# Kernel optimization log

Measured on AMD Instinct MI355X. Metric: run time of the kernel, lower is better.

Reference implementation:

```python
import jax, jax.numpy as jnp
import numpy as np

# ---- db4 filters (pywt conventions: dec_lo = rec_lo[::-1], rec_hi = qmf(rec_lo)) ----
F = 8  # db4 filter length
_rec_lo = np.array([0.23037781330885523, 0.7148465705525415, 0.6308807679295904,
                    -0.027983769416983849, -0.18703481171888114, 0.030841381835986965,
                    0.032883011666982945, -0.010597401784997278], dtype=np.float32)
_rec_hi = _rec_lo[::-1].copy()
_rec_hi[1::2] *= -1.0
REC_LO = jnp.asarray(_rec_lo)
REC_HI = jnp.asarray(_rec_hi)

MAX_LEVEL = 9  # pywt.dwt_max_level(4096, 8)


def _conv1d(x, kernel, stride=1, padding='VALID', lhs_dilation=None):
    # x: [B, L] -> correlation (XLA conv does NOT flip the kernel)
    out = jax.lax.conv_general_dilated(
        x[:, None, :], kernel[None, None, :],
        window_strides=(stride,), padding=padding,
        lhs_dilation=lhs_dilation,
        dimension_numbers=('NCH', 'OIH', 'NCH'))
    return out[:, 0, :]


def dwt(x):
    # pywt.dwt(x, 'db4', mode='symmetric'):
    # cA = np.convolve(sym_ext(x, F-1), dec_lo, 'valid')[1::2]
    # convolution with dec filter == correlation with rec filter (its reverse)
    ext = jnp.pad(x, ((0, 0), (F - 1, F - 1)), mode='symmetric')[:, 1:]
    return _conv1d(ext, REC_LO, stride=2), _conv1d(ext, REC_HI, stride=2)


def idwt(ca, cd):
    # pywt.idwt: zero-upsample coeffs, full convolution with rec filters, trim edges
    n = ca.shape[1]
    pad = ((F - 1, F - 1),)
    out = (_conv1d(ca, REC_LO[::-1], padding=pad, lhs_dilation=(2,)) +
           _conv1d(cd, REC_HI[::-1], padding=pad, lhs_dilation=(2,)))
    return out[:, F - 2:2 * n]  # output length = 2n - F + 2


def wavelet_features(x1):
    # Faithful to WaveletDWTLayer stack + WaveletParsingLayer: at each level k>=2,
    # reconstruct with details of levels k and k-1 only (others zeroed), with
    # pywt.waverec's trim-by-one rule; concatenate the 8 full-length reconstructions.
    a = x1
    cds, recs = [], []
    for level in range(1, MAX_LEVEL + 1):
        a, d = dwt(a)
        if level >= 2:
            r = idwt(jnp.zeros_like(d), d)
            for j in range(level - 2, -1, -1):
                dj = cds[j] if j == level - 2 else jnp.zeros_like(cds[j])
                if r.shape[1] == dj.shape[1] + 1:  # waverec trim rule
                    r = r[:, :-1]
                r = idwt(r, dj)
            recs.append(r)  # [B, signal_length]
        cds.append(d)
    return jnp.concatenate(recs, axis=1)  # [B, signal_length*(MAX_LEVEL-1)]


def reference(x1, x2, x3, W0, b0, W1, b1, W2, b2):
    # x2/x3 are placeholders in the original module (overwritten by layers 1/2)
    h = wavelet_features(x1)
    for W, b in ((W0, b0), (W1, b1), (W2, b2)):
        h = jax.nn.relu(h) @ W.T + b
    return h


def setup_inputs() -> dict:
    key = jax.random.key(0)
    ks = jax.random.split(key, 4)
    B, N = 2048, 4096
    D_IN, H1, H2, OUT = 32768, 181, 13, 10
    return {
        'x1': jax.random.normal(ks[0], (B, N), jnp.float32),
        'x2': jnp.zeros((B, 1, 8), jnp.float32),
        'x3': jnp.zeros((B, 1, 8), jnp.float32),
        'W0': jax.random.normal(ks[1], (H1, D_IN), jnp.float32) / np.float32(np.sqrt(D_IN)),
        'b0': jnp.zeros((H1,), jnp.float32),
        'W1': jax.random.normal(ks[2], (H2, H1), jnp.float32) / np.float32(np.sqrt(H1)),
        'b1': jnp.zeros((H2,), jnp.float32),
        'W2': jax.random.normal(ks[3], (OUT, H2), jnp.float32) / np.float32(np.sqrt(H2)),
        'b2': jnp.zeros((OUT,), jnp.float32),
    }
```

## Files before the change

kernel.cpp:

```cpp
#include <hip/hip_runtime.h>
#include <hip/hip_bf16.h>


typedef _Float16 f16x8 __attribute__((ext_vector_type(8)));
typedef _Float16 f16x4v __attribute__((ext_vector_type(4)));
typedef float f32x4 __attribute__((ext_vector_type(4)));

#define WV_THREADS 256
#define NSPLIT 32
#define KCHUNK 1024
#define GEMM_BM 256

#define L0 0.23037781330885523f
#define L1 0.7148465705525415f
#define L2f 0.6308807679295904f
#define L3 -0.02798376941698385f
#define L4 -0.18703481171888114f
#define L5 0.030841381835986965f
#define L6 0.032883011666982945f
#define L7 -0.010597401784997278f

#define H0 -0.010597401784997278f
#define H1 -0.032883011666982945f
#define H2 0.030841381835986965f
#define H3 0.18703481171888114f
#define H4 -0.02798376941698385f
#define H5 -0.6308807679295904f
#define H6 0.7148465705525415f
#define H7 -0.23037781330885523f

__constant__ constexpr int cNL[10] = {4096, 2051, 1029, 518, 262, 134, 70, 38, 22, 14};

__device__ __forceinline__ int ext_idx(int j, int n) {
  return (j < 6) ? (5 - j) : ((j < n + 6) ? (j - 6) : (2 * n + 5 - j));
}

__device__ __forceinline__ void dwt2(const float* a, float* anext, float* d,
                                     int n, int m, bool store_a) {
  const int ng = (m + 1) >> 1;
  for (int g = threadIdx.x; g < ng; g += WV_THREADS) {
    float w[10];
    if (g >= 2 && 4 * g + 9 <= n + 5) {
      const float2* af = (const float2*)a + (2 * g - 3);
      float2 b0 = af[0], b1 = af[1], b2 = af[2], b3 = af[3], b4 = af[4];
      w[0] = b0.x; w[1] = b0.y; w[2] = b1.x; w[3] = b1.y; w[4] = b2.x;
      w[5] = b2.y; w[6] = b3.x; w[7] = b3.y; w[8] = b4.x; w[9] = b4.y;
    } else {
#pragma unroll
      for (int q = 0; q < 10; ++q) {
        int j = 4 * g + q;
        int jm = n + 12;
        if (j > jm) j = jm;
        w[q] = a[ext_idx(j, n)];
      }
    }
    float sl0 = w[0]*L0 + w[1]*L1 + w[2]*L2f + w[3]*L3 + w[4]*L4 + w[5]*L5 + w[6]*L6 + w[7]*L7;
    float sh0 = w[0]*H0 + w[1]*H1 + w[2]*H2  + w[3]*H3 + w[4]*H4 + w[5]*H5 + w[6]*H6 + w[7]*H7;
    float sl1 = w[2]*L0 + w[3]*L1 + w[4]*L2f + w[5]*L3 + w[6]*L4 + w[7]*L5 + w[8]*L6 + w[9]*L7;
    float sh1 = w[2]*H0 + w[3]*H1 + w[4]*H2  + w[5]*H3 + w[6]*H4 + w[7]*H5 + w[8]*H6 + w[9]*H7;
    if (2 * g + 1 < m) {
      if (store_a) *(float2*)(anext + 2 * g) = make_float2(sl0, sl1);
      *(float2*)(d + 2 * g) = make_float2(sh0, sh1);
    } else {
      if (store_a) anext[2 * g] = sl0;
      d[2 * g] = sh0;
    }
  }
}

#define SWZ(u) ((u) ^ (((u) >> 3) & 7))
__device__ __forceinline__ const float4* lds4c(const float* b, int s) {
  return (const float4*)b + SWZ(s);
}
__device__ __forceinline__ float4* lds4(float* b, int s) {
  return (float4*)b + SWZ(s);
}

template <int NP>
__device__ __forceinline__ void lvlL(const float* a, float* v) {
#pragma unroll
  for (int q = 0; q < NP; ++q) {
    v[2*q]   = a[q+3]*L0 + a[q+2]*L2f + a[q+1]*L4 + a[q]*L6;
    v[2*q+1] = a[q+3]*L1 + a[q+2]*L3  + a[q+1]*L5 + a[q]*L7;
  }
}
template <int NP>
__device__ __forceinline__ void lvlH(const float* d, float* v) {
#pragma unroll
  for (int q = 0; q < NP; ++q) {
    v[2*q]   = d[q+3]*H0 + d[q+2]*H2 + d[q+1]*H4 + d[q]*H6;
    v[2*q+1] = d[q+3]*H1 + d[q+2]*H3 + d[q+1]*H5 + d[q]*H7;
  }
}
template <int NP>
__device__ __forceinline__ void lvlLH(const float* a, const float* d, float* v) {
#pragma unroll
  for (int q = 0; q < NP; ++q) {
    v[2*q]   = a[q+3]*L0 + a[q+2]*L2f + a[q+1]*L4 + a[q]*L6
             + d[q+3]*H0 + d[q+2]*H2  + d[q+1]*H4 + d[q]*H6;
    v[2*q+1] = a[q+3]*L1 + a[q+2]*L3  + a[q+1]*L5 + a[q]*L7
             + d[q+3]*H1 + d[q+2]*H3  + d[q+1]*H5 + d[q]*H7;
  }
}

__device__ __forceinline__ void g8f2(const float* p, int s, float* w) {
#pragma unroll
  for (int i = 0; i < 4; ++i) {
    float2 v = *(const float2*)(p + s + 2 * i);
    w[2*i] = v.x; w[2*i+1] = v.y;
  }
}
__device__ __forceinline__ void g12f4(const float* p, int s, float* w) {
#pragma unroll
  for (int i = 0; i < 3; ++i) {
    float4 v = *(const float4*)(p + s + 4 * i);
    w[4*i] = v.x; w[4*i+1] = v.y; w[4*i+2] = v.z; w[4*i+3] = v.w;
  }
}

__device__ __forceinline__ void store16(_Float16* outg, int t, const float* v) {
  f16x8 h0, h1;
#pragma unroll
  for (int i = 0; i < 8; ++i) h0[i] = (_Float16)fmaxf(v[i], 0.f);
#pragma unroll
  for (int i = 0; i < 8; ++i) h1[i] = (_Float16)fmaxf(v[8 + i], 0.f);
  *(f16x8*)(outg + 16 * t) = h0;
  *(f16x8*)(outg + 16 * t + 8) = h1;
}

__device__ __forceinline__ void fin2(const float* d2, const float* d1, _Float16* og) {
  const int t = threadIdx.x;
  float dw[12];  g12f4(d2, 4 * t, dw);
  float mid[12]; lvlH<6>(dw, mid);
  float d1w[12]; g12f4(d1, 8 * t, d1w);
  float v[16];   lvlLH<8>(mid, d1w, v);
  store16(og, t, v);
}

__device__ __forceinline__ void fin3(const float* d3, const float* d2, _Float16* og) {
  const int t = threadIdx.x;
  float dw[8];   g8f2(d3, 2 * t, dw);
  float v0[10];  lvlH<5>(dw, v0);
  float d2w[12]; g12f4(d2, 4 * t, d2w);
  float v1[12];  lvlLH<6>(v0, d2w, v1);
  float v[16];   lvlL<8>(v1, v);
  store16(og, t, v);
}

__device__ __forceinline__ void fin4(const float* d4, const float* d3, _Float16* og) {
  const int t = threadIdx.x;
  float dw[7];
#pragma unroll
  for (int i = 0; i < 7; ++i) dw[i] = d4[t + i];
  float v0[8];   lvlH<4>(dw, v0);
  float d3w[8];  g8f2(d3, 2 * t, d3w);
  float v1[10];  lvlLH<5>(v0, d3w, v1);
  float v2[12];  lvlL<6>(v1, v2);
  float v[16];   lvlL<8>(v2, v);
  store16(og, t, v);
}

template <bool FINAL, int N>
__device__ __forceinline__ void stepL(const float* ca, float* outl, _Float16* outg) {
  constexpr int npair = N - 3;
  constexpr int ng = (npair + 7) >> 3;
  const int t = threadIdx.x;
  if (t >= ng) return;
  float w[12];
  float4 a = *lds4c(ca, 2 * t), b = *lds4c(ca, 2 * t + 1), c = *lds4c(ca, 2 * t + 2);
  w[0]=a.x; w[1]=a.y; w[2]=a.z; w[3]=a.w; w[4]=b.x; w[5]=b.y; w[6]=b.z; w[7]=b.w;
  w[8]=c.x; w[9]=c.y; w[10]=c.z; w[11]=c.w;
  float v[16]; lvlL<8>(w, v);
  if constexpr (FINAL) {
    store16(outg, t, v);
  } else {
#pragma unroll
    for (int j = 0; j < 4; ++j) {
      const int p2 = 8 * t + 2 * j;
      if (p2 + 1 < npair) {
        *lds4(outl, 4 * t + j) = make_float4(v[4*j], v[4*j+1], v[4*j+2], v[4*j+3]);
      } else if (p2 < npair) {
        *(float2*)lds4(outl, 4 * t + j) = make_float2(v[4*j], v[4*j+1]);
      }
    }
  }
}

__device__ __forceinline__ void nocd2_core(const float w[12], float r[11],
                                           float E[8], float O[8]) {
#pragma unroll
  for (int h = 0; h < 6; ++h) {
    float e = w[h+3]*L0 + w[h+2]*L2f + w[h+1]*L4 + w[h]*L6;
    float o = w[h+3]*L1 + w[h+2]*L3  + w[h+1]*L5 + w[h]*L7;
    r[2*h] = e;
    if (2*h + 1 < 11) r[2*h+1] = o;
  }
#pragma unroll
  for (int pp = 0; pp < 8; ++pp) {
    E[pp] = r[pp+3]*L0 + r[pp+2]*L2f + r[pp+1]*L4 + r[pp]*L6;
    O[pp] = r[pp+3]*L1 + r[pp+2]*L3  + r[pp+1]*L5 + r[pp]*L7;
  }
}

template <int N1>
__device__ __forceinline__ void pair16(const float* cur, float* outl) {
  constexpr int N2 = (2 * N1 - 6 == 1030) ? 1029 : (2 * N1 - 6);
  constexpr int np2 = N2 - 3;
  constexpr int ng = (np2 + 7) >> 3;
  const int t = threadIdx.x;
  if (t >= ng) return;
  float w[12];
  float4 a = *lds4c(cur, t), b = *lds4c(cur, t + 1), c = *lds4c(cur, t + 2);
  w[0]=a.x; w[1]=a.y; w[2]=a.z; w[3]=a.w; w[4]=b.x; w[5]=b.y; w[6]=b.z; w[7]=b.w;
  w[8]=c.x; w[9]=c.y; w[10]=c.z; w[11]=c.w;
  float r[11], E[8], O[8];
  nocd2_core(w, r, E, O);
#pragma unroll
  for (int j = 0; j < 4; ++j) {
    const int p2 = 8 * t + 2 * j;
    if (p2 + 1 < np2) {
      *lds4(outl, 4 * t + j) = make_float4(E[2*j], O[2*j], E[2*j+1], O[2*j+1]);
    } else if (p2 < np2) {
      *(float2*)lds4(outl, 4 * t + j) = make_float2(E[2*j], O[2*j]);
    }
  }
}

__device__ __forceinline__ void finpair16(const float* cur, _Float16* outg) {
  const int t = threadIdx.x;
  float w[12];
  float4 a = *lds4c(cur, t), b = *lds4c(cur, t + 1), c = *lds4c(cur, t + 2);
  w[0]=a.x; w[1]=a.y; w[2]=a.z; w[3]=a.w; w[4]=b.x; w[5]=b.y; w[6]=b.z; w[7]=b.w;
  w[8]=c.x; w[9]=c.y; w[10]=c.z; w[11]=c.w;
  float r[11], E[8], O[8];
  nocd2_core(w, r, E, O);
  float vv[16];
#pragma unroll
  for (int q = 0; q < 8; ++q) { vv[2*q] = E[q]; vv[2*q+1] = O[q]; }
  store16(outg, t, vv);
}

template <int NL, int NLm1>
__device__ __forceinline__ void initpair16(const float* cdL, const float* cdm,
                                           float* outl) {
  constexpr int np2 = NLm1 - 3;
  constexpr int ng = (np2 + 7) >> 3;
  const int t = threadIdx.x;
  if (t >= ng) return;
  float w[12]; g12f4(cdL, 4 * t, w);
  float r[11];
#pragma unroll
  for (int h = 0; h < 6; ++h) {
    float e = w[h+3]*H0 + w[h+2]*H2 + w[h+1]*H4 + w[h]*H6;
    float o = w[h+3]*H1 + w[h+2]*H3 + w[h+1]*H5 + w[h]*H7;
    r[2*h] = e;
    if (2*h + 1 < 11) r[2*h+1] = o;
  }
  float v[12]; g12f4(cdm, 8 * t, v);
  float E[8], O[8];
#pragma unroll
  for (int pp = 0; pp < 8; ++pp) {
    E[pp] = r[pp+3]*L0 + r[pp+2]*L2f + r[pp+1]*L4 + r[pp]*L6
          + v[pp+3]*H0 + v[pp+2]*H2  + v[pp+1]*H4 + v[pp]*H6;
    O[pp] = r[pp+3]*L1 + r[pp+2]*L3  + r[pp+1]*L5 + r[pp]*L7
          + v[pp+3]*H1 + v[pp+2]*H3  + v[pp+1]*H5 + v[pp]*H7;
  }
#pragma unroll
  for (int j = 0; j < 4; ++j) {
    const int p2 = 8 * t + 2 * j;
    if (p2 + 1 < np2) {
      *lds4(outl, 4 * t + j) = make_float4(E[2*j], O[2*j], E[2*j+1], O[2*j+1]);
    } else if (p2 < np2) {
      *(float2*)lds4(outl, 4 * t + j) = make_float2(E[2*j], O[2*j]);
    }
  }
}

__global__ __launch_bounds__(WV_THREADS, 3) void wv_row_cvt(
    const float* __restrict__ x, _Float16* __restrict__ A,
    const float* __restrict__ W0, _Float16* __restrict__ Bw) {
  __shared__ alignas(16) float r1[4104];
  __shared__ alignas(16) float r2[2056];
  __shared__ alignas(16) float d1b[2052];
  __shared__ alignas(16) float s1[2080];
  __shared__ alignas(16) float s2[2080];
  const int tid = threadIdx.x;

  if (blockIdx.x >= 2048) {
    size_t i = ((size_t)(blockIdx.x - 2048) * 256 + tid) * 4;
    int rowc = (int)(i >> 15);
    f16x4v h;
    if (rowc < 181) {
      const float4 v = *(const float4*)(W0 + i);
      h[0] = (_Float16)v.x; h[1] = (_Float16)v.y;
      h[2] = (_Float16)v.z; h[3] = (_Float16)v.w;
    } else {
      h[0] = (_Float16)0.f; h[1] = (_Float16)0.f;
      h[2] = (_Float16)0.f; h[3] = (_Float16)0.f;
    }
    *(f16x4v*)(Bw + i) = h;
    return;
  }

  const int NLa[10]  = {4096, 2051, 1029, 518, 262, 134, 70, 38, 22, 14};
  const int LOFF[10] = {0, 0, 1036, 520, 2068, 1040, 2332, 1176, 2404, 1216};
  const int row = blockIdx.x;

  const float4* xr = (const float4*)(x + (size_t)row * 4096);
  for (int i = tid; i < 1024; i += WV_THREADS) ((float4*)r1)[i] = xr[i];
  __syncthreads();

  dwt2(r1, r2, d1b, NLa[0], NLa[1], true);
  __syncthreads();
  const float* ap = r2;
  float* an = r1;
  for (int lev = 2; lev <= 9; ++lev) {
    float* dbuf = ((lev & 1) ? r2 : r1) + LOFF[lev];
    dwt2(ap, an, dbuf, NLa[lev - 1], NLa[lev], lev < 9);
    __syncthreads();
    const float* t = ap; ap = an; an = (float*)t;
  }
  const float* d2 = r1 + 1036;  const float* d3 = r2 + 520;
  const float* d4 = r1 + 2068;  const float* d5 = r2 + 1040;
  const float* d6 = r1 + 2332;  const float* d7 = r2 + 1176;
  const float* d8 = r1 + 2404;  const float* d9 = r2 + 1216;

  _Float16* og = A + (size_t)row * 32768;

  fin2(d2, d1b, og);
  fin3(d3, d2, og + 4096);
  fin4(d4, d3, og + 8192);

  initpair16<cNL[5], cNL[4]>(d5, d4, s1);
  __syncthreads();
  pair16<518>(s1, s2); __syncthreads();
  stepL<true, 2051>(s2, nullptr, og + 3 * 4096);
  initpair16<cNL[6], cNL[5]>(d6, d5, s1);
  __syncthreads();
  pair16<262>(s1, s2); __syncthreads();
  finpair16(s2, og + 4 * 4096);
  initpair16<cNL[7], cNL[6]>(d7, d6, s1);
  __syncthreads();
  pair16<134>(s1, s2); __syncthreads();
  pair16<518>(s2, s1); __syncthreads();
  stepL<true, 2051>(s1, nullptr, og + 5 * 4096);
  initpair16<cNL[8], cNL[7]>(d8, d7, s1);
  __syncthreads();
  pair16<70>(s1, s2); __syncthreads();
  pair16<262>(s2, s1); __syncthreads();
  finpair16(s1, og + 6 * 4096);
  initpair16<cNL[9], cNL[8]>(d9, d8, s1);
  __syncthreads();
  pair16<38>(s1, s2); __syncthreads();
  pair16<134>(s2, s1); __syncthreads();
  pair16<518>(s1, s2); __syncthreads();
  stepL<true, 2051>(s2, nullptr, og + 7 * 4096);
}

__device__ __forceinline__ void load_lds16(const void* g, void* l) {
  __builtin_amdgcn_global_load_lds((__attribute__((address_space(1))) unsigned int*)g,
                                   (__attribute__((address_space(3))) unsigned int*)l,
                                   16, 0, 0);
}

__global__ __launch_bounds__(512, 2) void gemm_kernel(
    const _Float16* __restrict__ A, const _Float16* __restrict__ Bw,
    float* __restrict__ P) {
  __shared__ _Float16 As[2][GEMM_BM * 64];
  __shared__ _Float16 Bs[2][192 * 64];
  const int tid = threadIdx.x;
  const int lane = tid & 63;
  const int wave = tid >> 6;
  const int m0 = blockIdx.x * GEMM_BM;
  const int k_idx = blockIdx.y;
  const int k0 = k_idx * KCHUNK;

  f32x4 acc[2][12];
#pragma unroll
  for (int mt = 0; mt < 2; ++mt)
#pragma unroll
    for (int nt = 0; nt < 12; ++nt) acc[mt][nt] = (f32x4){0.f, 0.f, 0.f, 0.f};

  auto stage = [&](int ks, int b) {
    const int kbase = k0 + (ks << 6);
#pragma unroll
    for (int t = 0; t < 4; ++t) {
      int c = wave * 4 + t;
      int g = (c << 6) + lane;
      int r = g >> 3, cs = g & 7;
      const _Float16* gp = A + (size_t)(m0 + r) * 32768 + kbase + ((cs ^ (r & 7)) << 3);
      load_lds16(gp, (char*)As[b] + ((size_t)c << 10));
    }
#pragma unroll
    for (int t = 0; t < 3; ++t) {
      int c = wave * 3 + t;
      int g = (c << 6) + lane;
      int r = g >> 3, cs = g & 7;
      const _Float16* gp = Bw + (size_t)r * 32768 + kbase + ((cs ^ (r & 7)) << 3);
      load_lds16(gp, (char*)Bs[b] + ((size_t)c << 10));
    }
  };

  auto compute = [&](int cur) {
#pragma unroll
    for (int kk = 0; kk < 2; ++kk) {
      const int chunk = kk * 4 + (lane >> 4);
      f16x8 af[2];
#pragma unroll
      for (int mt = 0; mt < 2; ++mt) {
        int r = wave * 32 + mt * 16 + (lane & 15);
        af[mt] = *(const f16x8*)(As[cur] + r * 64 + ((chunk ^ (r & 7)) << 3));
      }
#pragma unroll
      for (int nt = 0; nt < 12; ++nt) {
        int rb = nt * 16 + (lane & 15);
        f16x8 bf = *(const f16x8*)(Bs[cur] + rb * 64 + ((chunk ^ (rb & 7)) << 3));
        acc[0][nt] = __builtin_amdgcn_mfma_f32_16x16x32_f16(af[0], bf, acc[0][nt], 0, 0, 0);
        acc[1][nt] = __builtin_amdgcn_mfma_f32_16x16x32_f16(af[1], bf, acc[1][nt], 0, 0, 0);
      }
    }
  };

  constexpr int NT = KCHUNK >> 6;
  stage(0, 0);
  for (int ks = 0; ks < NT - 1; ++ks) {
    stage(ks + 1, (ks + 1) & 1);
    asm volatile("s_waitcnt vmcnt(7)" ::: "memory");
    __builtin_amdgcn_s_barrier();
    compute(ks & 1);
    __builtin_amdgcn_s_barrier();
  }
  asm volatile("s_waitcnt vmcnt(0)" ::: "memory");
  __builtin_amdgcn_s_barrier();
  compute((NT - 1) & 1);

  float* Pp = P + ((size_t)k_idx * 2048 + m0) * 192;
#pragma unroll
  for (int mt = 0; mt < 2; ++mt)
#pragma unroll
    for (int nt = 0; nt < 12; ++nt)
#pragma unroll
      for (int r4 = 0; r4 < 4; ++r4) {
        int rr = wave * 32 + mt * 16 + ((lane >> 4) << 2) + r4;
        int cc = nt * 16 + (lane & 15);
        Pp[(size_t)rr * 192 + cc] = acc[mt][nt][r4];
      }
}

__global__ __launch_bounds__(256) void mlp_kernel(
    const float* __restrict__ P, const float* __restrict__ b0,
    const float* __restrict__ W1, const float* __restrict__ b1,
    const float* __restrict__ W2, const float* __restrict__ b2,
    float* __restrict__ out) {
  __shared__ float part[4][193];
  __shared__ float h1[192];
  __shared__ float h2[13];
  const int row = blockIdx.x;
  const int t = threadIdx.x;
  const int g = t >> 6;
  const int l = t & 63;

  float a0 = 0.f, a1 = 0.f, a2 = 0.f;
  for (int si = 0; si < NSPLIT / 4; ++si) {
    int s = g + (si << 2);
    const float* Pr = P + ((size_t)s * 2048 + row) * 192;
    a0 += Pr[l]; a1 += Pr[64 + l]; a2 += Pr[128 + l];
  }
  part[g][l] = a0; part[g][64 + l] = a1; part[g][128 + l] = a2;
  __syncthreads();

  if (t < 192) {
    float v = part[0][t] + part[1][t] + part[2][t] + part[3][t];
    h1[t] = (t < 181) ? fmaxf(v + b0[t], 0.f) : 0.f;
  }
  __syncthreads();

#pragma unroll
  for (int r = 0; r < 4; ++r) {
    int j = g + (r << 2);
    if (j < 13) {
      float v = 0.f;
#pragma unroll
      for (int q = 0; q < 3; ++q) {
        int n = l + (q << 6);
        if (n < 181) v += h1[n] * W1[j * 181 + n];
      }
      for (int off = 32; off >= 1; off >>= 1) v += __shfl_down(v, off);
      if (l == 0) h2[j] = fmaxf(v + b1[j], 0.f);
    }
  }
  __syncthreads();

  if (t < 10) {
    float c = b2[t];
#pragma unroll
    for (int j = 0; j < 13; ++j) c += h2[j] * W2[t * 13 + j];
    out[(size_t)row * 10 + t] = c;
  }
}

extern "C" void kernel_launch(void* const* d_in, const int* in_sizes, int n_in,
                              void* d_out, int out_size, void* d_ws, size_t ws_size,
                              hipStream_t stream) {
  const float* x1 = (const float*)d_in[0];
  const float* W0 = (const float*)d_in[3];
  const float* b0 = (const float*)d_in[4];
  const float* W1 = (const float*)d_in[5];
  const float* b1 = (const float*)d_in[6];
  const float* W2 = (const float*)d_in[7];
  const float* b2 = (const float*)d_in[8];
  float* out = (float*)d_out;

  char* ws = (char*)d_ws;
  const size_t A_BYTES = (size_t)2048 * 32768 * 2;
  const size_t B_BYTES = (size_t)192 * 32768 * 2;
  _Float16* Afeat = (_Float16*)ws;
  _Float16* Bw = (_Float16*)(ws + A_BYTES);
  float* P = (float*)(ws + A_BYTES + B_BYTES);

  wv_row_cvt<<<2048 + 6144, WV_THREADS, 0, stream>>>(x1, Afeat, W0, Bw);
  dim3 gg(2048 / GEMM_BM, NSPLIT);
  gemm_kernel<<<gg, 512, 0, stream>>>(Afeat, Bw, P);
  mlp_kernel<<<2048, 256, 0, stream>>>(P, b0, W1, b1, W2, b2, out);
}
```

Baseline: 236.4 us.

## Double wavelet block to 512 threads with 8 outputs per thread

Raises the wavelet/reconstruction block size from 256 to 512 threads and reworks every reconstruction stage so each thread produces 8 outputs instead of 16. The aim is more parallelism and lower register pressure per thread, so occupancy can rise (launch bounds go from 3 to 6). Extra __syncthreads are inserted between the final stores and the next initpair, and the W0 conversion grid is halved to match. In exchange there is more overlapping-window recomputation and more LDS reads per output.

```diff
diff --git a/kernel.cpp b/kernel.cpp
--- a/kernel.cpp
+++ b/kernel.cpp
@@ -6,7 +6,7 @@
 typedef _Float16 f16x4v __attribute__((ext_vector_type(4)));
 typedef float f32x4 __attribute__((ext_vector_type(4)));
 
-#define WV_THREADS 256
+#define WV_THREADS 512
 #define NSPLIT 32
 #define KCHUNK 1024
 #define GEMM_BM 256
@@ -28,8 +28,6 @@
 #define H5 -0.6308807679295904f
 #define H6 0.7148465705525415f
 #define H7 -0.23037781330885523f
-
-__constant__ constexpr int cNL[10] = {4096, 2051, 1029, 518, 262, 134, 70, 38, 22, 14};
 
 __device__ __forceinline__ int ext_idx(int j, int n) {
   return (j < 6) ? (5 - j) : ((j < n + 6) ? (j - 6) : (2 * n + 5 - j));
@@ -110,173 +108,118 @@
     w[2*i] = v.x; w[2*i+1] = v.y;
   }
 }
-__device__ __forceinline__ void g12f4(const float* p, int s, float* w) {
-#pragma unroll
-  for (int i = 0; i < 3; ++i) {
-    float4 v = *(const float4*)(p + s + 4 * i);
-    w[4*i] = v.x; w[4*i+1] = v.y; w[4*i+2] = v.z; w[4*i+3] = v.w;
-  }
-}
-
-__device__ __forceinline__ void store16(_Float16* outg, int t, const float* v) {
-  f16x8 h0, h1;
-#pragma unroll
-  for (int i = 0; i < 8; ++i) h0[i] = (_Float16)fmaxf(v[i], 0.f);
-#pragma unroll
-  for (int i = 0; i < 8; ++i) h1[i] = (_Float16)fmaxf(v[8 + i], 0.f);
-  *(f16x8*)(outg + 16 * t) = h0;
-  *(f16x8*)(outg + 16 * t + 8) = h1;
+__device__ __forceinline__ void g7s(const float* p, int s, float* w) {
+#pragma unroll
+  for (int i = 0; i < 7; ++i) w[i] = p[s + i];
+}
+
+__device__ __forceinline__ void store8(_Float16* outg, int t, const float* v) {
+  f16x8 h;
+#pragma unroll
+  for (int i = 0; i < 8; ++i) h[i] = (_Float16)fmaxf(v[i], 0.f);
+  *(f16x8*)(outg + 8 * t) = h;
+}
+
+template <int NP2>
+__device__ __forceinline__ void wr8(float* outl, int t, const float* v8) {
+  if (4 * t + 1 < NP2) {
+    *lds4(outl, 2 * t) = make_float4(v8[0], v8[1], v8[2], v8[3]);
+  } else if (4 * t < NP2) {
+    *(float2*)lds4(outl, 2 * t) = make_float2(v8[0], v8[1]);
+  }
+  if (4 * t + 3 < NP2) {
+    *lds4(outl, 2 * t + 1) = make_float4(v8[4], v8[5], v8[6], v8[7]);
+  } else if (4 * t + 2 < NP2) {
+    *(float2*)lds4(outl, 2 * t + 1) = make_float2(v8[4], v8[5]);
+  }
+}
+
+__device__ __forceinline__ void ldwin12(const float* s, int t, float* w12) {
+  const int h = t >> 1;
+  float4 a = *lds4c(s, h), b = *lds4c(s, h + 1), c = *lds4c(s, h + 2);
+  w12[0]=a.x; w12[1]=a.y; w12[2]=a.z; w12[3]=a.w;
+  w12[4]=b.x; w12[5]=b.y; w12[6]=b.z; w12[7]=b.w;
+  w12[8]=c.x; w12[9]=c.y; w12[10]=c.z; w12[11]=c.w;
 }
 
 __device__ __forceinline__ void fin2(const float* d2, const float* d1, _Float16* og) {
   const int t = threadIdx.x;
-  float dw[12];  g12f4(d2, 4 * t, dw);
-  float mid[12]; lvlH<6>(dw, mid);
-  float d1w[12]; g12f4(d1, 8 * t, d1w);
-  float v[16];   lvlLH<8>(mid, d1w, v);
-  store16(og, t, v);
+  float dw[8];  g8f2(d2, 2 * t, dw);
+  float m8[8];  lvlH<4>(dw, m8);
+  float d1w[8]; g8f2(d1, 4 * t, d1w);
+  float v[8];   lvlLH<4>(m8, d1w, v);
+  store8(og, t, v);
 }
 
 __device__ __forceinline__ void fin3(const float* d3, const float* d2, _Float16* og) {
   const int t = threadIdx.x;
-  float dw[8];   g8f2(d3, 2 * t, dw);
-  float v0[10];  lvlH<5>(dw, v0);
-  float d2w[12]; g12f4(d2, 4 * t, d2w);
-  float v1[12];  lvlLH<6>(v0, d2w, v1);
-  float v[16];   lvlL<8>(v1, v);
-  store16(og, t, v);
+  float dw[7];  g7s(d3, t, dw);
+  float v0[8];  lvlH<4>(dw, v0);
+  float d2w[8]; g8f2(d2, 2 * t, d2w);
+  float w1[8];  lvlLH<4>(v0, d2w, w1);
+  float v[8];   lvlL<4>(w1, v);
+  store8(og, t, v);
 }
 
 __device__ __forceinline__ void fin4(const float* d4, const float* d3, _Float16* og) {
   const int t = threadIdx.x;
-  float dw[7];
-#pragma unroll
-  for (int i = 0; i < 7; ++i) dw[i] = d4[t + i];
-  float v0[8];   lvlH<4>(dw, v0);
-  float d3w[8];  g8f2(d3, 2 * t, d3w);
-  float v1[10];  lvlLH<5>(v0, d3w, v1);
-  float v2[12];  lvlL<6>(v1, v2);
-  float v[16];   lvlL<8>(v2, v);
-  store16(og, t, v);
-}
-
-template <bool FINAL, int N>
-__device__ __forceinline__ void stepL(const float* ca, float* outl, _Float16* outg) {
-  constexpr int npair = N - 3;
-  constexpr int ng = (npair + 7) >> 3;
+  const int u = t >> 1;
+  float dw[7];  g7s(d4, u, dw);
+  float i8[8];  lvlH<4>(dw, i8);
+  float d3w[7]; g7s(d3, t, d3w);
+  float w1[8];  lvlLH<4>(i8 + (t & 1), d3w, w1);
+  float w2[8];  lvlL<4>(w1, w2);
+  float v[8];   lvlL<4>(w2, v);
+  store8(og, t, v);
+}
+
+__device__ __forceinline__ void final8(const float* s, _Float16* og) {
+  const int t = threadIdx.x;
+  float w[8];
+  float4 a = *lds4c(s, t), b = *lds4c(s, t + 1);
+  w[0]=a.x; w[1]=a.y; w[2]=a.z; w[3]=a.w; w[4]=b.x; w[5]=b.y; w[6]=b.z; w[7]=b.w;
+  float v[8]; lvlL<4>(w, v);
+  store8(og, t, v);
+}
+
+__device__ __forceinline__ void finpair8(const float* s, _Float16* og) {
+  const int t = threadIdx.x;
+  float w12[12]; ldwin12(s, t, w12);
+  const float* w = w12 + ((t & 1) << 1);
+  float r[8]; lvlL<4>(w, r);
+  float v[8]; lvlL<4>(r, v);
+  store8(og, t, v);
+}
+
+template <int N1>
+__device__ __forceinline__ void pair8(const float* cur, float* outl) {
+  constexpr int N2 = (2 * N1 - 6 == 1030) ? 1029 : (2 * N1 - 6);
+  constexpr int NP2 = N2 - 3;
+  constexpr int ng = (NP2 + 3) >> 2;
   const int t = threadIdx.x;
   if (t >= ng) return;
-  float w[12];
-  float4 a = *lds4c(ca, 2 * t), b = *lds4c(ca, 2 * t + 1), c = *lds4c(ca, 2 * t + 2);
-  w[0]=a.x; w[1]=a.y; w[2]=a.z; w[3]=a.w; w[4]=b.x; w[5]=b.y; w[6]=b.z; w[7]=b.w;
-  w[8]=c.x; w[9]=c.y; w[10]=c.z; w[11]=c.w;
-  float v[16]; lvlL<8>(w, v);
-  if constexpr (FINAL) {
-    store16(outg, t, v);
-  } else {
-#pragma unroll
-    for (int j = 0; j < 4; ++j) {
-      const int p2 = 8 * t + 2 * j;
-      if (p2 + 1 < npair) {
-        *lds4(outl, 4 * t + j) = make_float4(v[4*j], v[4*j+1], v[4*j+2], v[4*j+3]);
-      } else if (p2 < npair) {
-        *(float2*)lds4(outl, 4 * t + j) = make_float2(v[4*j], v[4*j+1]);
-      }
-    }
-  }
-}
-
-__device__ __forceinline__ void nocd2_core(const float w[12], float r[11],
-                                           float E[8], float O[8]) {
-#pragma unroll
-  for (int h = 0; h < 6; ++h) {
-    float e = w[h+3]*L0 + w[h+2]*L2f + w[h+1]*L4 + w[h]*L6;
-    float o = w[h+3]*L1 + w[h+2]*L3  + w[h+1]*L5 + w[h]*L7;
-    r[2*h] = e;
-    if (2*h + 1 < 11) r[2*h+1] = o;
-  }
-#pragma unroll
-  for (int pp = 0; pp < 8; ++pp) {
-    E[pp] = r[pp+3]*L0 + r[pp+2]*L2f + r[pp+1]*L4 + r[pp]*L6;
-    O[pp] = r[pp+3]*L1 + r[pp+2]*L3  + r[pp+1]*L5 + r[pp]*L7;
-  }
-}
-
-template <int N1>
-__device__ __forceinline__ void pair16(const float* cur, float* outl) {
-  constexpr int N2 = (2 * N1 - 6 == 1030) ? 1029 : (2 * N1 - 6);
-  constexpr int np2 = N2 - 3;
-  constexpr int ng = (np2 + 7) >> 3;
+  float w12[12]; ldwin12(cur, t, w12);
+  const float* w = w12 + ((t & 1) << 1);
+  float r[8]; lvlL<4>(w, r);
+  float v[8]; lvlL<4>(r, v);
+  wr8<NP2>(outl, t, v);
+}
+
+template <int NLm1>
+__device__ __forceinline__ void initpair8(const float* dL, const float* dm,
+                                          float* outl) {
+  constexpr int NP2 = NLm1 - 3;
+  constexpr int ng = (NP2 + 3) >> 2;
   const int t = threadIdx.x;
   if (t >= ng) return;
-  float w[12];
-  float4 a = *lds4c(cur, t), b = *lds4c(cur, t + 1), c = *lds4c(cur, t + 2);
-  w[0]=a.x; w[1]=a.y; w[2]=a.z; w[3]=a.w; w[4]=b.x; w[5]=b.y; w[6]=b.z; w[7]=b.w;
-  w[8]=c.x; w[9]=c.y; w[10]=c.z; w[11]=c.w;
-  float r[11], E[8], O[8];
-  nocd2_core(w, r, E, O);
-#pragma unroll
-  for (int j = 0; j < 4; ++j) {
-    const int p2 = 8 * t + 2 * j;
-    if (p2 + 1 < np2) {
-      *lds4(outl, 4 * t + j) = make_float4(E[2*j], O[2*j], E[2*j+1], O[2*j+1]);
-    } else if (p2 < np2) {
-      *(float2*)lds4(outl, 4 * t + j) = make_float2(E[2*j], O[2*j]);
-    }
-  }
-}
-
-__device__ __forceinline__ void finpair16(const float* cur, _Float16* outg) {
-  const int t = threadIdx.x;
-  float w[12];
-  float4 a = *lds4c(cur, t), b = *lds4c(cur, t + 1), c = *lds4c(cur, t + 2);
-  w[0]=a.x; w[1]=a.y; w[2]=a.z; w[3]=a.w; w[4]=b.x; w[5]=b.y; w[6]=b.z; w[7]=b.w;
-  w[8]=c.x; w[9]=c.y; w[10]=c.z; w[11]=c.w;
-  float r[11], E[8], O[8];
-  nocd2_core(w, r, E, O);
-  float vv[16];
-#pragma unroll
-  for (int q = 0; q < 8; ++q) { vv[2*q] = E[q]; vv[2*q+1] = O[q]; }
-  store16(outg, t, vv);
-}
-
-template <int NL, int NLm1>
-__device__ __forceinline__ void initpair16(const float* cdL, const float* cdm,
-                                           float* outl) {
-  constexpr int np2 = NLm1 - 3;
-  constexpr int ng = (np2 + 7) >> 3;
-  const int t = threadIdx.x;
-  if (t >= ng) return;
-  float w[12]; g12f4(cdL, 4 * t, w);
-  float r[11];
-#pragma unroll
-  for (int h = 0; h < 6; ++h) {
-    float e = w[h+3]*H0 + w[h+2]*H2 + w[h+1]*H4 + w[h]*H6;
-    float o = w[h+3]*H1 + w[h+2]*H3 + w[h+1]*H5 + w[h]*H7;
-    r[2*h] = e;
-    if (2*h + 1 < 11) r[2*h+1] = o;
-  }
-  float v[12]; g12f4(cdm, 8 * t, v);
-  float E[8], O[8];
-#pragma unroll
-  for (int pp = 0; pp < 8; ++pp) {
-    E[pp] = r[pp+3]*L0 + r[pp+2]*L2f + r[pp+1]*L4 + r[pp]*L6
-          + v[pp+3]*H0 + v[pp+2]*H2  + v[pp+1]*H4 + v[pp]*H6;
-    O[pp] = r[pp+3]*L1 + r[pp+2]*L3  + r[pp+1]*L5 + r[pp]*L7
-          + v[pp+3]*H1 + v[pp+2]*H3  + v[pp+1]*H5 + v[pp]*H7;
-  }
-#pragma unroll
-  for (int j = 0; j < 4; ++j) {
-    const int p2 = 8 * t + 2 * j;
-    if (p2 + 1 < np2) {
-      *lds4(outl, 4 * t + j) = make_float4(E[2*j], O[2*j], E[2*j+1], O[2*j+1]);
-    } else if (p2 < np2) {
-      *(float2*)lds4(outl, 4 * t + j) = make_float2(E[2*j], O[2*j]);
-    }
-  }
-}
-
-__global__ __launch_bounds__(WV_THREADS, 3) void wv_row_cvt(
+  float dw[8]; g8f2(dL, 2 * t, dw);
+  float r[8];  lvlH<4>(dw, r);
+  float vm[8]; g8f2(dm, 4 * t, vm);
+  float v[8];  lvlLH<4>(r, vm, v);
+  wr8<NP2>(outl, t, v);
+}
+
+__global__ __launch_bounds__(WV_THREADS, 6) void wv_row_cvt(
     const float* __restrict__ x, _Float16* __restrict__ A,
     const float* __restrict__ W0, _Float16* __restrict__ Bw) {
   __shared__ alignas(16) float r1[4104];
@@ -287,7 +230,7 @@
   const int tid = threadIdx.x;
 
   if (blockIdx.x >= 2048) {
-    size_t i = ((size_t)(blockIdx.x - 2048) * 256 + tid) * 4;
+    size_t i = ((size_t)(blockIdx.x - 2048) * WV_THREADS + tid) * 4;
     int rowc = (int)(i >> 15);
     f16x4v h;
     if (rowc < 181) {
@@ -331,30 +274,34 @@
   fin3(d3, d2, og + 4096);
   fin4(d4, d3, og + 8192);
 
-  initpair16<cNL[5], cNL[4]>(d5, d4, s1);
-  __syncthreads();
-  pair16<518>(s1, s2); __syncthreads();
-  stepL<true, 2051>(s2, nullptr, og + 3 * 4096);
-  initpair16<cNL[6], cNL[5]>(d6, d5, s1);
-  __syncthreads();
-  pair16<262>(s1, s2); __syncthreads();
-  finpair16(s2, og + 4 * 4096);
-  initpair16<cNL[7], cNL[6]>(d7, d6, s1);
-  __syncthreads();
-  pair16<134>(s1, s2); __syncthreads();
-  pair16<518>(s2, s1); __syncthreads();
-  stepL<true, 2051>(s1, nullptr, og + 5 * 4096);
-  initpair16<cNL[8], cNL[7]>(d8, d7, s1);
-  __syncthreads();
-  pair16<70>(s1, s2); __syncthreads();
-  pair16<262>(s2, s1); __syncthreads();
-  finpair16(s1, og + 6 * 4096);
-  initpair16<cNL[9], cNL[8]>(d9, d8, s1);
-  __syncthreads();
-  pair16<38>(s1, s2); __syncthreads();
-  pair16<134>(s2, s1); __syncthreads();
-  pair16<518>(s1, s2); __syncthreads();
-  stepL<true, 2051>(s2, nullptr, og + 7 * 4096);
+  initpair8<262>(d5, d4, s1);
+  __syncthreads();
+  pair8<518>(s1, s2); __syncthreads();
+  final8(s2, og + 3 * 4096);
+  __syncthreads();
+  initpair8<134>(d6, d5, s1);
+  __syncthreads();
+  pair8<262>(s1, s2); __syncthreads();
+  finpair8(s2, og + 4 * 4096);
+  __syncthreads();
+  initpair8<70>(d7, d6, s1);
+  __syncthreads();
+  pair8<134>(s1, s2); __syncthreads();
+  pair8<518>(s2, s1); __syncthreads();
+  final8(s1, og + 5 * 4096);
+  __syncthreads();
+  initpair8<38>(d8, d7, s1);
+  __syncthreads();
+  pair8<70>(s1, s2); __syncthreads();
+  pair8<262>(s2, s1); __syncthreads();
+  finpair8(s1, og + 6 * 4096);
+  __syncthreads();
+  initpair8<22>(d9, d8, s1);
+  __syncthreads();
+  pair8<38>(s1, s2); __syncthreads();
+  pair8<134>(s2, s1); __syncthreads();
+  pair8<518>(s1, s2); __syncthreads();
+  final8(s2, og + 7 * 4096);
 }
 
 __device__ __forceinline__ void load_lds16(const void* g, void* l) {
@@ -518,7 +465,7 @@
   _Float16* Bw = (_Float16*)(ws + A_BYTES);
   float* P = (float*)(ws + A_BYTES + B_BYTES);
 
-  wv_row_cvt<<<2048 + 6144, WV_THREADS, 0, stream>>>(x1, Afeat, W0, Bw);
+  wv_row_cvt<<<2048 + 3072, WV_THREADS, 0, stream>>>(x1, Afeat, W0, Bw);
   dim3 gg(2048 / GEMM_BM, NSPLIT);
   gemm_kernel<<<gg, 512, 0, stream>>>(Afeat, Bw, P);
   mlp_kernel<<<2048, 256, 0, stream>>>(P, b0, W1, b1, W2, b2, out);
```

New measurement: 243.5 us. 3.0% more time.
